# Kernel optimization log

Measured on AMD Instinct MI355X. Metric: run time of the kernel, lower is better.

The kernel has to match this reference:

```python
import jax, jax.numpy as jnp
import numpy as np

JITTER_EPS = 0.01  # router_jitter_noise


def sparsemixer_top2(scores, jitter_eps):
    # scores: [T, E]. Faithful port of PhiMoE sparsemixer (top_k == 2).
    E = scores.shape[-1]
    eye = jnp.arange(E)
    # ---- expert 1 ----
    max1 = jnp.max(scores, axis=-1, keepdims=True)
    ind1 = jnp.argmax(scores, axis=-1)                      # [T]
    factor1 = jnp.maximum(jnp.abs(scores), max1)            # scores.abs().clamp(min=max)
    mask1 = (max1 - scores) / factor1 > 2.0 * jitter_eps
    gates1 = jax.nn.softmax(jnp.where(mask1, -jnp.inf, scores), axis=-1)
    mult1 = jnp.take_along_axis(gates1, ind1[:, None], axis=-1)   # [T,1]
    # ---- expert 2: mask out first pick, repeat ----
    oh1 = eye[None, :] == ind1[:, None]
    masked_scores = jnp.where(oh1, -jnp.inf, scores)
    max2 = jnp.max(masked_scores, axis=-1, keepdims=True)
    ind2 = jnp.argmax(masked_scores, axis=-1)
    factor2 = jnp.maximum(jnp.abs(scores), max2)
    mask2 = (max2 - scores) / factor2 > 2.0 * jitter_eps
    gates2 = jax.nn.softmax(jnp.where(mask2, -jnp.inf, masked_scores), axis=-1)
    mult2 = jnp.take_along_axis(gates2, ind2[:, None], axis=-1)   # [T,1]
    topk_w = jnp.concatenate([mult1, mult2], axis=-1)       # [T,2]
    topk_ids = jnp.stack([ind1, ind2], axis=-1)             # [T,2]
    return topk_w, topk_ids


def setup_inputs() -> dict:
    key = jax.random.key(0)
    ks = jax.random.split(key, 5)
    B, S, D, F, E = 2, 2048, 1024, 2048, 8
    hidden_states = jax.random.normal(ks[0], (B, S, D), dtype=jnp.float32)
    gate_w = jax.random.normal(ks[1], (E, D), dtype=jnp.float32) * (D ** -0.5)
    w_gate = jax.random.normal(ks[2], (E, F, D), dtype=jnp.float32) * (D ** -0.5)
    w_up = jax.random.normal(ks[3], (E, F, D), dtype=jnp.float32) * (D ** -0.5)
    w_down = jax.random.normal(ks[4], (E, D, F), dtype=jnp.float32) * (F ** -0.5)
    return {"hidden_states": hidden_states, "gate_w": gate_w,
            "w_gate": w_gate, "w_up": w_up, "w_down": w_down}


def reference(hidden_states, gate_w, w_gate, w_up, w_down):
    B, S, D = hidden_states.shape
    E = gate_w.shape[0]
    x = hidden_states.reshape(-1, D)                         # [T,D]
    router_logits = x @ gate_w.T                             # [T,E]
    topk_w, topk_ids = sparsemixer_top2(router_logits, JITTER_EPS)
    # per-token combine weights over experts: [T,E]
    comb = jnp.sum(topk_w[:, :, None] *
                   (topk_ids[:, :, None] == jnp.arange(E)[None, None, :]).astype(topk_w.dtype),
                   axis=1)
    out = jnp.zeros_like(x)
    for e in range(E):  # small fixed expert count
        h = jax.nn.silu(x @ w_gate[e].T) * (x @ w_up[e].T)   # [T,F]
        out = out + comb[:, e:e + 1] * (h @ w_down[e].T)     # [T,D]
    return out.reshape(B, S, D), router_logits
```

## Files before the change

kernel.cpp:

```cpp
#include <hip/hip_runtime.h>
#include <stdint.h>

#define TOK    4096
#define DMODEL 1024
#define FDIM   2048
#define NEXP   8
#define MAXP   9216
#define MAXT   72
#define OUT_MAIN (TOK * DMODEL)

#define IDX_NT  24
#define IDX_TE  32
#define IDX_TR  112

#define OFF_META 0
#define OFF_TKW  33792
#define OFF_PTOK 66560
#define OFF_PW   103424
#define OFF_XG   140288
#define OFF_H    19014656
#define OFF_WGB  56763392
#define OFF_WUB  90317824
#define OFF_WDB  123872256
#define OFF_PV   OFF_WGB
#define OFF_RPOS 157426688
#define WS_NEED  157459456

typedef __attribute__((ext_vector_type(8)))  __bf16 bf16x8;
typedef __attribute__((ext_vector_type(8)))  unsigned short u16x8;
typedef __attribute__((ext_vector_type(4)))  unsigned short u16x4;
typedef __attribute__((ext_vector_type(16))) float f32x16;

__device__ __forceinline__ unsigned short f2bf(float f) {
  unsigned u = __builtin_bit_cast(unsigned, f);
  u += 0x7fffu + ((u >> 16) & 1u);
  return (unsigned short)(u >> 16);
}

__device__ __forceinline__ void async_load16(const void* g, void* l) {
  __builtin_amdgcn_global_load_lds(
      (__attribute__((address_space(1))) void*)g,
      (__attribute__((address_space(3))) void*)l, 16, 0, 0);
}

__device__ __forceinline__ bf16x8 ld_frag(const unsigned short* p) {
  return __builtin_bit_cast(bf16x8, *(const u16x8*)p);
}

__global__ void k_prep(const float* __restrict__ wg, const float* __restrict__ wu,
                       const float* __restrict__ wd, unsigned short* __restrict__ wgb,
                       unsigned short* __restrict__ wub, unsigned short* __restrict__ wdb,
                       const float* __restrict__ x, const float* __restrict__ gw,
                       float* __restrict__ logits, int pre) {
  int b = blockIdx.x;
  if (b < 24576) {
    if (!pre) return;
    const float* src; unsigned short* dst; int bb;
    if (b < 8192)       { src = wg; dst = wgb; bb = b; }
    else if (b < 16384) { src = wu; dst = wub; bb = b - 8192; }
    else                { src = wd; dst = wdb; bb = b - 16384; }
    size_t i = ((size_t)bb * 256 + threadIdx.x) * 8;
    float4 a = *(const float4*)(src + i);
    float4 c = *(const float4*)(src + i + 4);
    u16x8 v = {f2bf(a.x), f2bf(a.y), f2bf(a.z), f2bf(a.w),
               f2bf(c.x), f2bf(c.y), f2bf(c.z), f2bf(c.w)};
    *(u16x8*)(dst + i) = v;
    return;
  }
  int lane = threadIdx.x & 63;
  int t = (b - 24576) * 4 + (threadIdx.x >> 6);
  double acc[NEXP];
#pragma unroll
  for (int e = 0; e < NEXP; ++e) acc[e] = 0.0;
  const float* xp = x + (size_t)t * DMODEL;
  for (int i = 0; i < DMODEL / 64; ++i) {
    int d = i * 64 + lane;
    float xv = xp[d];
#pragma unroll
    for (int e = 0; e < NEXP; ++e) acc[e] += (double)xv * (double)gw[e * DMODEL + d];
  }
#pragma unroll
  for (int e = 0; e < NEXP; ++e) {
    double v = acc[e];
#pragma unroll
    for (int off = 32; off > 0; off >>= 1) v += __shfl_down(v, off, 64);
    if (lane == 0) logits[t * NEXP + e] = (float)v;
  }
}

__global__ __launch_bounds__(1024) void k_route2(
    const float* __restrict__ logits, int* __restrict__ meta,
    float* __restrict__ tk_w, int* __restrict__ ptok, float* __restrict__ pw,
    int* __restrict__ rpos) {
  __shared__ int cnt[NEXP], cur[NEXP], seg[NEXP];
  int tid = threadIdx.x;
  if (tid < NEXP) { cnt[tid] = 0; cur[tid] = 0; }
  for (int r = tid; r < MAXP; r += 1024) ptok[r] = -1;
  __syncthreads();
  int i1[4], i2[4]; float w1v[4], w2v[4];
#pragma unroll
  for (int j = 0; j < 4; ++j) {
    int t = tid + j * 1024;
    float s[NEXP];
#pragma unroll
    for (int e = 0; e < NEXP; ++e) s[e] = logits[t * NEXP + e];
    float max1 = s[0]; int ind1 = 0;
#pragma unroll
    for (int e = 1; e < NEXP; ++e) if (s[e] > max1) { max1 = s[e]; ind1 = e; }
    float sum1 = 0.f;
#pragma unroll
    for (int e = 0; e < NEXP; ++e) {
      float f = fmaxf(fabsf(s[e]), max1);
      if (!((max1 - s[e]) / f > 0.02f)) sum1 += expf(s[e] - max1);
    }
    float max2 = -3.4e38f; int ind2 = 0;
#pragma unroll
    for (int e = 0; e < NEXP; ++e) if (e != ind1 && s[e] > max2) { max2 = s[e]; ind2 = e; }
    float sum2 = 0.f;
#pragma unroll
    for (int e = 0; e < NEXP; ++e) {
      if (e == ind1) continue;
      float f = fmaxf(fabsf(s[e]), max2);
      if (!((max2 - s[e]) / f > 0.02f)) sum2 += expf(s[e] - max2);
    }
    i1[j] = ind1; i2[j] = ind2; w1v[j] = 1.f / sum1; w2v[j] = 1.f / sum2;
    atomicAdd(&cnt[ind1], 1);
    atomicAdd(&cnt[ind2], 1);
  }
  __syncthreads();
  if (tid == 0) {
    int off = 0, nt2 = 0;
    for (int e = 0; e < NEXP; ++e) {
      seg[e] = off;
      int tiles = (cnt[e] + 127) >> 7;
      for (int j = 0; j < tiles; ++j) {
        meta[IDX_TE + nt2] = e;
        meta[IDX_TR + nt2] = off + (j << 7);
        ++nt2;
      }
      off += tiles << 7;
    }
    meta[IDX_NT] = nt2;
  }
  __syncthreads();
#pragma unroll
  for (int j = 0; j < 4; ++j) {
    int t = tid + j * 1024;
    int e1 = i1[j];
    int p1 = atomicAdd(&cur[e1], 1);
    int r1 = seg[e1] + p1;
    ptok[r1] = t; pw[r1] = w1v[j]; rpos[2 * t] = r1; tk_w[2 * t] = w1v[j];
    int e2 = i2[j];
    int p2 = atomicAdd(&cur[e2], 1);
    int r2 = seg[e2] + p2;
    ptok[r2] = t; pw[r2] = w2v[j]; rpos[2 * t + 1] = r2; tk_w[2 * t + 1] = w2v[j];
  }
}

__global__ void k_gather(const float* __restrict__ x, const int* __restrict__ ptok,
                         unsigned short* __restrict__ xg) {
  int r = blockIdx.x;
  int t = ptok[r];
  int c = threadIdx.x << 2;
  unsigned short o0 = 0, o1 = 0, o2 = 0, o3 = 0;
  if (t >= 0) {
    float4 v = *(const float4*)(x + ((size_t)t << 10) + c);
    o0 = f2bf(v.x); o1 = f2bf(v.y); o2 = f2bf(v.z); o3 = f2bf(v.w);
  }
  u16x4 o = {o0, o1, o2, o3};
  *(u16x4*)(xg + ((size_t)r << 10) + c) = o;
}

template <bool PRE>
__global__ __launch_bounds__(256, 4) void k_gu(
    const unsigned short* __restrict__ xg,
    const float* __restrict__ wg32, const float* __restrict__ wu32,
    const unsigned short* __restrict__ wgb, const unsigned short* __restrict__ wub,
    unsigned short* __restrict__ h, const int* __restrict__ meta) {
  int nt = meta[IDX_NT];
  int rt = blockIdx.y;
  if (rt >= nt) return;
  int e = meta[IDX_TE + rt];
  int row0 = meta[IDX_TR + rt];
  int n0 = blockIdx.x * 64;

  __shared__ __align__(16) unsigned short As[8192], Bg[4096], Bu[4096];

  int tid = threadIdx.x, lane = tid & 63, w = tid >> 6;
  int wm = w & 1, wn = w >> 1;
  int l31 = lane & 31, lh = lane >> 5;

  f32x16 accg[2], accu[2];
#pragma unroll
  for (int i = 0; i < 2; ++i) {
#pragma unroll
    for (int r = 0; r < 16; ++r) { accg[i][r] = 0.f; accu[i][r] = 0.f; }
  }

  const unsigned short* Abase =
      xg + (size_t)(row0 + w * 32 + l31) * DMODEL + lh * 8;
  int c0 = w * 2, c1 = c0 + 1;
  const unsigned short* G0; const unsigned short* G1;
  const unsigned short* U0; const unsigned short* U1;
  if constexpr (PRE) {
    const unsigned short* WgB = wgb + (size_t)e * FDIM * DMODEL;
    const unsigned short* WuB = wub + (size_t)e * FDIM * DMODEL;
    size_t o0 = (size_t)(n0 + ((c0 >> 2) << 5) + l31) * DMODEL + ((c0 & 3) << 4) + lh * 8;
    size_t o1 = (size_t)(n0 + ((c1 >> 2) << 5) + l31) * DMODEL + ((c1 & 3) << 4) + lh * 8;
    G0 = WgB + o0; G1 = WgB + o1; U0 = WuB + o0; U1 = WuB + o1;
  }

  for (int ks = 0; ks < DMODEL / 64; ++ks) {
    int k0 = ks * 64;
    if (ks) __syncthreads();
    async_load16(Abase + k0,      &As[(w * 4 + 0) * 512]);
    async_load16(Abase + k0 + 16, &As[(w * 4 + 1) * 512]);
    async_load16(Abase + k0 + 32, &As[(w * 4 + 2) * 512]);
    async_load16(Abase + k0 + 48, &As[(w * 4 + 3) * 512]);
    if constexpr (PRE) {
      async_load16(G0 + k0, &Bg[c0 * 512]);
      async_load16(G1 + k0, &Bg[c1 * 512]);
      async_load16(U0 + k0, &Bu[c0 * 512]);
      async_load16(U1 + k0, &Bu[c1 * 512]);
    } else {
      const float* Wg = wg32 + (size_t)e * FDIM * DMODEL;
      const float* Wu = wu32 + (size_t)e * FDIM * DMODEL;
#pragma unroll
      for (int i2 = 0; i2 < 2; ++i2) {
        int tau = tid + 256 * i2;
        int c = tau >> 6, l = tau & 63;
        int nrow = n0 + ((c >> 2) << 5) + (l & 31);
        int kk = k0 + ((c & 3) << 4) + ((l >> 5) << 3);
        const float* sg = Wg + (size_t)nrow * DMODEL + kk;
        const float* su = Wu + (size_t)nrow * DMODEL + kk;
        float4 g0 = *(const float4*)sg;
        float4 g1 = *(const float4*)(sg + 4);
        float4 u0 = *(const float4*)su;
        float4 u1 = *(const float4*)(su + 4);
        u16x8 vg = {f2bf(g0.x), f2bf(g0.y), f2bf(g0.z), f2bf(g0.w),
                    f2bf(g1.x), f2bf(g1.y), f2bf(g1.z), f2bf(g1.w)};
        u16x8 vu = {f2bf(u0.x), f2bf(u0.y), f2bf(u0.z), f2bf(u0.w),
                    f2bf(u1.x), f2bf(u1.y), f2bf(u1.z), f2bf(u1.w)};
        *(u16x8*)&Bg[c * 512 + l * 8] = vg;
        *(u16x8*)&Bu[c * 512 + l * 8] = vu;
      }
    }
    __syncthreads();
#pragma unroll
    for (int kq = 0; kq < 4; ++kq) {
      bf16x8 a0 = ld_frag(&As[((wm * 2 + 0) * 4 + kq) * 512 + lane * 8]);
      bf16x8 a1 = ld_frag(&As[((wm * 2 + 1) * 4 + kq) * 512 + lane * 8]);
      bf16x8 vg = ld_frag(&Bg[(wn * 4 + kq) * 512 + lane * 8]);
      bf16x8 vu = ld_frag(&Bu[(wn * 4 + kq) * 512 + lane * 8]);
      accg[0] = __builtin_amdgcn_mfma_f32_32x32x16_bf16(a0, vg, accg[0], 0, 0, 0);
      accg[1] = __builtin_amdgcn_mfma_f32_32x32x16_bf16(a1, vg, accg[1], 0, 0, 0);
      accu[0] = __builtin_amdgcn_mfma_f32_32x32x16_bf16(a0, vu, accu[0], 0, 0, 0);
      accu[1] = __builtin_amdgcn_mfma_f32_32x32x16_bf16(a1, vu, accu[1], 0, 0, 0);
    }
  }
  int col = n0 + wn * 32 + l31;
#pragma unroll
  for (int mt = 0; mt < 2; ++mt) {
#pragma unroll
    for (int r = 0; r < 16; ++r) {
      int lrow = wm * 64 + mt * 32 + (r & 3) + ((r >> 2) << 3) + lh * 4;
      float gv = accg[mt][r], uv = accu[mt][r];
      float hv = gv * uv / (1.f + __expf(-gv));
      h[(size_t)(row0 + lrow) * FDIM + col] = f2bf(hv);
    }
  }
}

template <bool PRE>
__global__ __launch_bounds__(256, 5) void k_down(
    const unsigned short* __restrict__ h, const float* __restrict__ wd32,
    const unsigned short* __restrict__ wdb, float* __restrict__ out,
    float* __restrict__ pv, const int* __restrict__ meta,
    const int* __restrict__ ptok, const float* __restrict__ pw) {
  int nt = meta[IDX_NT];
  int rt = blockIdx.y;
  if (rt >= nt) return;
  int e = meta[IDX_TE + rt];
  int row0 = meta[IDX_TR + rt];
  int d0 = blockIdx.x * 64;

  __shared__ __align__(16) unsigned short Ah[8192], Bd[4096];
  __shared__ int stok[128];
  __shared__ float sw[128];

  int tid = threadIdx.x, lane = tid & 63, w = tid >> 6;
  int wm = w & 1, wn = w >> 1;
  int l31 = lane & 31, lh = lane >> 5;

  if constexpr (!PRE) {
    if (tid < 128) { stok[tid] = ptok[row0 + tid]; sw[tid] = pw[row0 + tid]; }
  }

  f32x16 acc[2];
#pragma unroll
  for (int i = 0; i < 2; ++i) {
#pragma unroll
    for (int r = 0; r < 16; ++r) acc[i][r] = 0.f;
  }

  const unsigned short* Abase =
      h + (size_t)(row0 + w * 32 + l31) * FDIM + lh * 8;
  int c0 = w * 2, c1 = c0 + 1;
  const unsigned short* D0; const unsigned short* D1;
  if constexpr (PRE) {
    const unsigned short* WdB = wdb + (size_t)e * DMODEL * FDIM;
    D0 = WdB + (size_t)(d0 + ((c0 >> 2) << 5) + l31) * FDIM + ((c0 & 3) << 4) + lh * 8;
    D1 = WdB + (size_t)(d0 + ((c1 >> 2) << 5) + l31) * FDIM + ((c1 & 3) << 4) + lh * 8;
  }

  for (int ks = 0; ks < FDIM / 64; ++ks) {
    int k0 = ks * 64;
    if (ks) __syncthreads();
    async_load16(Abase + k0,      &Ah[(w * 4 + 0) * 512]);
    async_load16(Abase + k0 + 16, &Ah[(w * 4 + 1) * 512]);
    async_load16(Abase + k0 + 32, &Ah[(w * 4 + 2) * 512]);
    async_load16(Abase + k0 + 48, &Ah[(w * 4 + 3) * 512]);
    if constexpr (PRE) {
      async_load16(D0 + k0, &Bd[c0 * 512]);
      async_load16(D1 + k0, &Bd[c1 * 512]);
    } else {
      const float* Wd = wd32 + (size_t)e * DMODEL * FDIM;
#pragma unroll
      for (int i2 = 0; i2 < 2; ++i2) {
        int tau = tid + 256 * i2;
        int c = tau >> 6, l = tau & 63;
        int drow = d0 + ((c >> 2) << 5) + (l & 31);
        int kk = k0 + ((c & 3) << 4) + ((l >> 5) << 3);
        const float* sd = Wd + (size_t)drow * FDIM + kk;
        float4 b0 = *(const float4*)sd;
        float4 b1 = *(const float4*)(sd + 4);
        u16x8 vb = {f2bf(b0.x), f2bf(b0.y), f2bf(b0.z), f2bf(b0.w),
                    f2bf(b1.x), f2bf(b1.y), f2bf(b1.z), f2bf(b1.w)};
        *(u16x8*)&Bd[c * 512 + l * 8] = vb;
      }
    }
    __syncthreads();
#pragma unroll
    for (int kq = 0; kq < 4; ++kq) {
      bf16x8 a0 = ld_frag(&Ah[((wm * 2 + 0) * 4 + kq) * 512 + lane * 8]);
      bf16x8 a1 = ld_frag(&Ah[((wm * 2 + 1) * 4 + kq) * 512 + lane * 8]);
      bf16x8 vb = ld_frag(&Bd[(wn * 4 + kq) * 512 + lane * 8]);
      acc[0] = __builtin_amdgcn_mfma_f32_32x32x16_bf16(a0, vb, acc[0], 0, 0, 0);
      acc[1] = __builtin_amdgcn_mfma_f32_32x32x16_bf16(a1, vb, acc[1], 0, 0, 0);
    }
  }
  int col = d0 + wn * 32 + l31;
#pragma unroll
  for (int mt = 0; mt < 2; ++mt) {
#pragma unroll
    for (int r = 0; r < 16; ++r) {
      int lrow = wm * 64 + mt * 32 + (r & 3) + ((r >> 2) << 3) + lh * 4;
      if constexpr (PRE) {
        pv[(size_t)(row0 + lrow) * DMODEL + col] = acc[mt][r];
      } else {
        int t = stok[lrow];
        if (t >= 0) atomicAdd(&out[(size_t)t * DMODEL + col], acc[mt][r] * sw[lrow]);
      }
    }
  }
}

__global__ void k_combine(const float* __restrict__ pv, const int* __restrict__ rpos,
                          const float* __restrict__ tkw, float* __restrict__ out) {
  int t = blockIdx.x;
  int r1 = rpos[2 * t], r2 = rpos[2 * t + 1];
  float w1 = tkw[2 * t], w2 = tkw[2 * t + 1];
  int c = threadIdx.x << 2;
  float4 a = *(const float4*)(pv + (size_t)r1 * DMODEL + c);
  float4 b = *(const float4*)(pv + (size_t)r2 * DMODEL + c);
  float4 o;
  o.x = w1 * a.x + w2 * b.x;
  o.y = w1 * a.y + w2 * b.y;
  o.z = w1 * a.z + w2 * b.z;
  o.w = w1 * a.w + w2 * b.w;
  *(float4*)(out + (size_t)t * DMODEL + c) = o;
}

extern "C" void kernel_launch(void* const* d_in, const int* in_sizes, int n_in,
                              void* d_out, int out_size, void* d_ws, size_t ws_size,
                              hipStream_t stream) {
  const float* x  = (const float*)d_in[0];
  const float* gw = (const float*)d_in[1];
  const float* wg = (const float*)d_in[2];
  const float* wu = (const float*)d_in[3];
  const float* wd = (const float*)d_in[4];
  float* out = (float*)d_out;
  float* logits = out + OUT_MAIN;

  char* wsb = (char*)d_ws;
  int* meta = (int*)(wsb + OFF_META);
  float* tk_w = (float*)(wsb + OFF_TKW);
  int* ptok = (int*)(wsb + OFF_PTOK);
  float* pw = (float*)(wsb + OFF_PW);
  unsigned short* xg = (unsigned short*)(wsb + OFF_XG);
  unsigned short* h = (unsigned short*)(wsb + OFF_H);
  unsigned short* wgb = (unsigned short*)(wsb + OFF_WGB);
  unsigned short* wub = (unsigned short*)(wsb + OFF_WUB);
  unsigned short* wdb = (unsigned short*)(wsb + OFF_WDB);
  float* pv = (float*)(wsb + OFF_PV);
  int* rpos = (int*)(wsb + OFF_RPOS);

  bool pre = ws_size >= (size_t)WS_NEED;
  if (!pre) hipMemsetAsync(out, 0, (size_t)OUT_MAIN * sizeof(float), stream);

  k_prep<<<25600, 256, 0, stream>>>(wg, wu, wd, wgb, wub, wdb, x, gw, logits, (int)pre);
  k_route2<<<1, 1024, 0, stream>>>(logits, meta, tk_w, ptok, pw, rpos);
  k_gather<<<MAXP, 256, 0, stream>>>(x, ptok, xg);
  if (pre) {
    k_gu<true><<<dim3(FDIM / 64, MAXT), 256, 0, stream>>>(xg, wg, wu, wgb, wub, h, meta);
    k_down<true><<<dim3(DMODEL / 64, MAXT), 256, 0, stream>>>(h, wd, wdb, out, pv, meta, ptok, pw);
    k_combine<<<TOK, 256, 0, stream>>>(pv, rpos, tk_w, out);
  } else {
    k_gu<false><<<dim3(FDIM / 64, MAXT), 256, 0, stream>>>(xg, wg, wu, wgb, wub, h, meta);
    k_down<false><<<dim3(DMODEL / 64, MAXT), 256, 0, stream>>>(h, wd, wdb, out, pv, meta, ptok, pw);
  }
}
```

Measured before the change: 519.2 us.

## Enlarge MoE GEMM tiles to 256x128 with 512-thread blocks and double-buffered LDS

The gate/up and down expert GEMMs move from 128x64 tiles with 256 threads to 256x128 tiles with 512 threads. Each wave now holds four M sub-tiles, which raises operand reuse per LDS fragment. The K loop is double-buffered so the next slab's async loads overlap the current MFMA work. Routing now pads each expert segment to multiples of 256 rows, so the workspace layout and MAXP/MAXT change to match. In exchange there is more padded work per expert, and the larger LDS footprint (about 128KB for gate/up) likely limits each CU to one block.

```diff
diff --git a/kernel.cpp b/kernel.cpp
--- a/kernel.cpp
+++ b/kernel.cpp
@@ -5,8 +5,8 @@
 #define DMODEL 1024
 #define FDIM   2048
 #define NEXP   8
-#define MAXP   9216
-#define MAXT   72
+#define MAXP   10240
+#define MAXT   40
 #define OUT_MAIN (TOK * DMODEL)
 
 #define IDX_NT  24
@@ -16,15 +16,15 @@
 #define OFF_META 0
 #define OFF_TKW  33792
 #define OFF_PTOK 66560
-#define OFF_PW   103424
-#define OFF_XG   140288
-#define OFF_H    19014656
-#define OFF_WGB  56763392
-#define OFF_WUB  90317824
-#define OFF_WDB  123872256
+#define OFF_PW   107520
+#define OFF_XG   148480
+#define OFF_H    21120000
+#define OFF_WGB  63063040
+#define OFF_WUB  96617472
+#define OFF_WDB  130171904
 #define OFF_PV   OFF_WGB
-#define OFF_RPOS 157426688
-#define WS_NEED  157459456
+#define OFF_RPOS 163726336
+#define WS_NEED  163759104
 
 typedef __attribute__((ext_vector_type(8)))  __bf16 bf16x8;
 typedef __attribute__((ext_vector_type(8)))  unsigned short u16x8;
@@ -132,13 +132,13 @@
     int off = 0, nt2 = 0;
     for (int e = 0; e < NEXP; ++e) {
       seg[e] = off;
-      int tiles = (cnt[e] + 127) >> 7;
+      int tiles = (cnt[e] + 255) >> 8;
       for (int j = 0; j < tiles; ++j) {
         meta[IDX_TE + nt2] = e;
-        meta[IDX_TR + nt2] = off + (j << 7);
+        meta[IDX_TR + nt2] = off + (j << 8);
         ++nt2;
       }
-      off += tiles << 7;
+      off += tiles << 8;
     }
     meta[IDX_NT] = nt2;
   }
@@ -172,7 +172,7 @@
 }
 
 template <bool PRE>
-__global__ __launch_bounds__(256, 4) void k_gu(
+__global__ __launch_bounds__(512, 2) void k_gu(
     const unsigned short* __restrict__ xg,
     const float* __restrict__ wg32, const float* __restrict__ wu32,
     const unsigned short* __restrict__ wgb, const unsigned short* __restrict__ wub,
@@ -182,52 +182,55 @@
   if (rt >= nt) return;
   int e = meta[IDX_TE + rt];
   int row0 = meta[IDX_TR + rt];
-  int n0 = blockIdx.x * 64;
-
-  __shared__ __align__(16) unsigned short As[8192], Bg[4096], Bu[4096];
+  int n0 = blockIdx.x * 128;
+
+  __shared__ __align__(16) unsigned short sA[2][16384];
+  __shared__ __align__(16) unsigned short sBg[2][8192];
+  __shared__ __align__(16) unsigned short sBu[2][8192];
 
   int tid = threadIdx.x, lane = tid & 63, w = tid >> 6;
   int wm = w & 1, wn = w >> 1;
   int l31 = lane & 31, lh = lane >> 5;
 
-  f32x16 accg[2], accu[2];
-#pragma unroll
-  for (int i = 0; i < 2; ++i) {
-#pragma unroll
-    for (int r = 0; r < 16; ++r) { accg[i][r] = 0.f; accu[i][r] = 0.f; }
+  f32x16 accg[4], accu[4];
+#pragma unroll
+  for (int m = 0; m < 4; ++m) {
+#pragma unroll
+    for (int r = 0; r < 16; ++r) { accg[m][r] = 0.f; accu[m][r] = 0.f; }
   }
 
   const unsigned short* Abase =
       xg + (size_t)(row0 + w * 32 + l31) * DMODEL + lh * 8;
-  int c0 = w * 2, c1 = c0 + 1;
-  const unsigned short* G0; const unsigned short* G1;
-  const unsigned short* U0; const unsigned short* U1;
+  int cb0 = w * 2, cb1 = cb0 + 1;
+  const unsigned short *G0, *G1, *U0, *U1;
   if constexpr (PRE) {
     const unsigned short* WgB = wgb + (size_t)e * FDIM * DMODEL;
     const unsigned short* WuB = wub + (size_t)e * FDIM * DMODEL;
-    size_t o0 = (size_t)(n0 + ((c0 >> 2) << 5) + l31) * DMODEL + ((c0 & 3) << 4) + lh * 8;
-    size_t o1 = (size_t)(n0 + ((c1 >> 2) << 5) + l31) * DMODEL + ((c1 & 3) << 4) + lh * 8;
+    size_t o0 = (size_t)(n0 + ((cb0 >> 2) << 5) + l31) * DMODEL + ((cb0 & 3) << 4) + lh * 8;
+    size_t o1 = (size_t)(n0 + ((cb1 >> 2) << 5) + l31) * DMODEL + ((cb1 & 3) << 4) + lh * 8;
     G0 = WgB + o0; G1 = WgB + o1; U0 = WuB + o0; U1 = WuB + o1;
   }
-
-  for (int ks = 0; ks < DMODEL / 64; ++ks) {
+  const float* Wg = nullptr; const float* Wu = nullptr;
+  if constexpr (!PRE) {
+    Wg = wg32 + (size_t)e * FDIM * DMODEL;
+    Wu = wu32 + (size_t)e * FDIM * DMODEL;
+  }
+
+  auto stage = [&](int buf, int ks) {
     int k0 = ks * 64;
-    if (ks) __syncthreads();
-    async_load16(Abase + k0,      &As[(w * 4 + 0) * 512]);
-    async_load16(Abase + k0 + 16, &As[(w * 4 + 1) * 512]);
-    async_load16(Abase + k0 + 32, &As[(w * 4 + 2) * 512]);
-    async_load16(Abase + k0 + 48, &As[(w * 4 + 3) * 512]);
+    async_load16(Abase + k0,      &sA[buf][(w * 4 + 0) * 512]);
+    async_load16(Abase + k0 + 16, &sA[buf][(w * 4 + 1) * 512]);
+    async_load16(Abase + k0 + 32, &sA[buf][(w * 4 + 2) * 512]);
+    async_load16(Abase + k0 + 48, &sA[buf][(w * 4 + 3) * 512]);
     if constexpr (PRE) {
-      async_load16(G0 + k0, &Bg[c0 * 512]);
-      async_load16(G1 + k0, &Bg[c1 * 512]);
-      async_load16(U0 + k0, &Bu[c0 * 512]);
-      async_load16(U1 + k0, &Bu[c1 * 512]);
+      async_load16(G0 + k0, &sBg[buf][cb0 * 512]);
+      async_load16(G1 + k0, &sBg[buf][cb1 * 512]);
+      async_load16(U0 + k0, &sBu[buf][cb0 * 512]);
+      async_load16(U1 + k0, &sBu[buf][cb1 * 512]);
     } else {
-      const float* Wg = wg32 + (size_t)e * FDIM * DMODEL;
-      const float* Wu = wu32 + (size_t)e * FDIM * DMODEL;
 #pragma unroll
       for (int i2 = 0; i2 < 2; ++i2) {
-        int tau = tid + 256 * i2;
+        int tau = tid + 512 * i2;
         int c = tau >> 6, l = tau & 63;
         int nrow = n0 + ((c >> 2) << 5) + (l & 31);
         int kk = k0 + ((c & 3) << 4) + ((l >> 5) << 3);
@@ -241,30 +244,49 @@
                     f2bf(g1.x), f2bf(g1.y), f2bf(g1.z), f2bf(g1.w)};
         u16x8 vu = {f2bf(u0.x), f2bf(u0.y), f2bf(u0.z), f2bf(u0.w),
                     f2bf(u1.x), f2bf(u1.y), f2bf(u1.z), f2bf(u1.w)};
-        *(u16x8*)&Bg[c * 512 + l * 8] = vg;
-        *(u16x8*)&Bu[c * 512 + l * 8] = vu;
+        *(u16x8*)&sBg[buf][c * 512 + l * 8] = vg;
+        *(u16x8*)&sBu[buf][c * 512 + l * 8] = vu;
       }
     }
-    __syncthreads();
+  };
+
+  auto compute = [&](int buf) {
 #pragma unroll
     for (int kq = 0; kq < 4; ++kq) {
-      bf16x8 a0 = ld_frag(&As[((wm * 2 + 0) * 4 + kq) * 512 + lane * 8]);
-      bf16x8 a1 = ld_frag(&As[((wm * 2 + 1) * 4 + kq) * 512 + lane * 8]);
-      bf16x8 vg = ld_frag(&Bg[(wn * 4 + kq) * 512 + lane * 8]);
-      bf16x8 vu = ld_frag(&Bu[(wn * 4 + kq) * 512 + lane * 8]);
+      bf16x8 a0 = ld_frag(&sA[buf][((wm * 4 + 0) * 4 + kq) * 512 + lane * 8]);
+      bf16x8 a1 = ld_frag(&sA[buf][((wm * 4 + 1) * 4 + kq) * 512 + lane * 8]);
+      bf16x8 a2 = ld_frag(&sA[buf][((wm * 4 + 2) * 4 + kq) * 512 + lane * 8]);
+      bf16x8 a3 = ld_frag(&sA[buf][((wm * 4 + 3) * 4 + kq) * 512 + lane * 8]);
+      bf16x8 vg = ld_frag(&sBg[buf][(wn * 4 + kq) * 512 + lane * 8]);
+      bf16x8 vu = ld_frag(&sBu[buf][(wn * 4 + kq) * 512 + lane * 8]);
       accg[0] = __builtin_amdgcn_mfma_f32_32x32x16_bf16(a0, vg, accg[0], 0, 0, 0);
       accg[1] = __builtin_amdgcn_mfma_f32_32x32x16_bf16(a1, vg, accg[1], 0, 0, 0);
+      accg[2] = __builtin_amdgcn_mfma_f32_32x32x16_bf16(a2, vg, accg[2], 0, 0, 0);
+      accg[3] = __builtin_amdgcn_mfma_f32_32x32x16_bf16(a3, vg, accg[3], 0, 0, 0);
       accu[0] = __builtin_amdgcn_mfma_f32_32x32x16_bf16(a0, vu, accu[0], 0, 0, 0);
       accu[1] = __builtin_amdgcn_mfma_f32_32x32x16_bf16(a1, vu, accu[1], 0, 0, 0);
-    }
-  }
+      accu[2] = __builtin_amdgcn_mfma_f32_32x32x16_bf16(a2, vu, accu[2], 0, 0, 0);
+      accu[3] = __builtin_amdgcn_mfma_f32_32x32x16_bf16(a3, vu, accu[3], 0, 0, 0);
+    }
+  };
+
+  stage(0, 0);
+  __syncthreads();
+  int cur = 0;
+  for (int ks = 0; ks < DMODEL / 64; ++ks) {
+    if (ks + 1 < DMODEL / 64) stage(cur ^ 1, ks + 1);
+    compute(cur);
+    __syncthreads();
+    cur ^= 1;
+  }
+
   int col = n0 + wn * 32 + l31;
 #pragma unroll
-  for (int mt = 0; mt < 2; ++mt) {
+  for (int m = 0; m < 4; ++m) {
 #pragma unroll
     for (int r = 0; r < 16; ++r) {
-      int lrow = wm * 64 + mt * 32 + (r & 3) + ((r >> 2) << 3) + lh * 4;
-      float gv = accg[mt][r], uv = accu[mt][r];
+      int lrow = wm * 128 + m * 32 + (r & 3) + ((r >> 2) << 3) + lh * 4;
+      float gv = accg[m][r], uv = accu[m][r];
       float hv = gv * uv / (1.f + __expf(-gv));
       h[(size_t)(row0 + lrow) * FDIM + col] = f2bf(hv);
     }
@@ -272,7 +294,7 @@
 }
 
 template <bool PRE>
-__global__ __launch_bounds__(256, 5) void k_down(
+__global__ __launch_bounds__(512, 2) void k_down(
     const unsigned short* __restrict__ h, const float* __restrict__ wd32,
     const unsigned short* __restrict__ wdb, float* __restrict__ out,
     float* __restrict__ pv, const int* __restrict__ meta,
@@ -282,52 +304,53 @@
   if (rt >= nt) return;
   int e = meta[IDX_TE + rt];
   int row0 = meta[IDX_TR + rt];
-  int d0 = blockIdx.x * 64;
-
-  __shared__ __align__(16) unsigned short Ah[8192], Bd[4096];
-  __shared__ int stok[128];
-  __shared__ float sw[128];
+  int d0 = blockIdx.x * 128;
+
+  __shared__ __align__(16) unsigned short sA[2][16384];
+  __shared__ __align__(16) unsigned short sB[2][8192];
+  __shared__ int stok[256];
+  __shared__ float sw_[256];
 
   int tid = threadIdx.x, lane = tid & 63, w = tid >> 6;
   int wm = w & 1, wn = w >> 1;
   int l31 = lane & 31, lh = lane >> 5;
 
   if constexpr (!PRE) {
-    if (tid < 128) { stok[tid] = ptok[row0 + tid]; sw[tid] = pw[row0 + tid]; }
-  }
-
-  f32x16 acc[2];
-#pragma unroll
-  for (int i = 0; i < 2; ++i) {
-#pragma unroll
-    for (int r = 0; r < 16; ++r) acc[i][r] = 0.f;
+    if (tid < 256) { stok[tid] = ptok[row0 + tid]; sw_[tid] = pw[row0 + tid]; }
+  }
+
+  f32x16 acc[4];
+#pragma unroll
+  for (int m = 0; m < 4; ++m) {
+#pragma unroll
+    for (int r = 0; r < 16; ++r) acc[m][r] = 0.f;
   }
 
   const unsigned short* Abase =
       h + (size_t)(row0 + w * 32 + l31) * FDIM + lh * 8;
-  int c0 = w * 2, c1 = c0 + 1;
-  const unsigned short* D0; const unsigned short* D1;
+  int cb0 = w * 2, cb1 = cb0 + 1;
+  const unsigned short *D0, *D1;
   if constexpr (PRE) {
     const unsigned short* WdB = wdb + (size_t)e * DMODEL * FDIM;
-    D0 = WdB + (size_t)(d0 + ((c0 >> 2) << 5) + l31) * FDIM + ((c0 & 3) << 4) + lh * 8;
-    D1 = WdB + (size_t)(d0 + ((c1 >> 2) << 5) + l31) * FDIM + ((c1 & 3) << 4) + lh * 8;
-  }
-
-  for (int ks = 0; ks < FDIM / 64; ++ks) {
+    D0 = WdB + (size_t)(d0 + ((cb0 >> 2) << 5) + l31) * FDIM + ((cb0 & 3) << 4) + lh * 8;
+    D1 = WdB + (size_t)(d0 + ((cb1 >> 2) << 5) + l31) * FDIM + ((cb1 & 3) << 4) + lh * 8;
+  }
+  const float* Wd = nullptr;
+  if constexpr (!PRE) Wd = wd32 + (size_t)e * DMODEL * FDIM;
+
+  auto stage = [&](int buf, int ks) {
     int k0 = ks * 64;
-    if (ks) __syncthreads();
-    async_load16(Abase + k0,      &Ah[(w * 4 + 0) * 512]);
-    async_load16(Abase + k0 + 16, &Ah[(w * 4 + 1) * 512]);
-    async_load16(Abase + k0 + 32, &Ah[(w * 4 + 2) * 512]);
-    async_load16(Abase + k0 + 48, &Ah[(w * 4 + 3) * 512]);
+    async_load16(Abase + k0,      &sA[buf][(w * 4 + 0) * 512]);
+    async_load16(Abase + k0 + 16, &sA[buf][(w * 4 + 1) * 512]);
+    async_load16(Abase + k0 + 32, &sA[buf][(w * 4 + 2) * 512]);
+    async_load16(Abase + k0 + 48, &sA[buf][(w * 4 + 3) * 512]);
     if constexpr (PRE) {
-      async_load16(D0 + k0, &Bd[c0 * 512]);
-      async_load16(D1 + k0, &Bd[c1 * 512]);
+      async_load16(D0 + k0, &sB[buf][cb0 * 512]);
+      async_load16(D1 + k0, &sB[buf][cb1 * 512]);
     } else {
-      const float* Wd = wd32 + (size_t)e * DMODEL * FDIM;
 #pragma unroll
       for (int i2 = 0; i2 < 2; ++i2) {
-        int tau = tid + 256 * i2;
+        int tau = tid + 512 * i2;
         int c = tau >> 6, l = tau & 63;
         int drow = d0 + ((c >> 2) << 5) + (l & 31);
         int kk = k0 + ((c & 3) << 4) + ((l >> 5) << 3);
@@ -336,30 +359,47 @@
         float4 b1 = *(const float4*)(sd + 4);
         u16x8 vb = {f2bf(b0.x), f2bf(b0.y), f2bf(b0.z), f2bf(b0.w),
                     f2bf(b1.x), f2bf(b1.y), f2bf(b1.z), f2bf(b1.w)};
-        *(u16x8*)&Bd[c * 512 + l * 8] = vb;
+        *(u16x8*)&sB[buf][c * 512 + l * 8] = vb;
       }
     }
-    __syncthreads();
+  };
+
+  auto compute = [&](int buf) {
 #pragma unroll
     for (int kq = 0; kq < 4; ++kq) {
-      bf16x8 a0 = ld_frag(&Ah[((wm * 2 + 0) * 4 + kq) * 512 + lane * 8]);
-      bf16x8 a1 = ld_frag(&Ah[((wm * 2 + 1) * 4 + kq) * 512 + lane * 8]);
-      bf16x8 vb = ld_frag(&Bd[(wn * 4 + kq) * 512 + lane * 8]);
+      bf16x8 a0 = ld_frag(&sA[buf][((wm * 4 + 0) * 4 + kq) * 512 + lane * 8]);
+      bf16x8 a1 = ld_frag(&sA[buf][((wm * 4 + 1) * 4 + kq) * 512 + lane * 8]);
+      bf16x8 a2 = ld_frag(&sA[buf][((wm * 4 + 2) * 4 + kq) * 512 + lane * 8]);
+      bf16x8 a3 = ld_frag(&sA[buf][((wm * 4 + 3) * 4 + kq) * 512 + lane * 8]);
+      bf16x8 vb = ld_frag(&sB[buf][(wn * 4 + kq) * 512 + lane * 8]);
       acc[0] = __builtin_amdgcn_mfma_f32_32x32x16_bf16(a0, vb, acc[0], 0, 0, 0);
       acc[1] = __builtin_amdgcn_mfma_f32_32x32x16_bf16(a1, vb, acc[1], 0, 0, 0);
-    }
-  }
+      acc[2] = __builtin_amdgcn_mfma_f32_32x32x16_bf16(a2, vb, acc[2], 0, 0, 0);
+      acc[3] = __builtin_amdgcn_mfma_f32_32x32x16_bf16(a3, vb, acc[3], 0, 0, 0);
+    }
+  };
+
+  stage(0, 0);
+  __syncthreads();
+  int cur = 0;
+  for (int ks = 0; ks < FDIM / 64; ++ks) {
+    if (ks + 1 < FDIM / 64) stage(cur ^ 1, ks + 1);
+    compute(cur);
+    __syncthreads();
+    cur ^= 1;
+  }
+
   int col = d0 + wn * 32 + l31;
 #pragma unroll
-  for (int mt = 0; mt < 2; ++mt) {
+  for (int m = 0; m < 4; ++m) {
 #pragma unroll
     for (int r = 0; r < 16; ++r) {
-      int lrow = wm * 64 + mt * 32 + (r & 3) + ((r >> 2) << 3) + lh * 4;
+      int lrow = wm * 128 + m * 32 + (r & 3) + ((r >> 2) << 3) + lh * 4;
       if constexpr (PRE) {
-        pv[(size_t)(row0 + lrow) * DMODEL + col] = acc[mt][r];
+        pv[(size_t)(row0 + lrow) * DMODEL + col] = acc[m][r];
       } else {
         int t = stok[lrow];
-        if (t >= 0) atomicAdd(&out[(size_t)t * DMODEL + col], acc[mt][r] * sw[lrow]);
+        if (t >= 0) atomicAdd(&out[(size_t)t * DMODEL + col], acc[m][r] * sw_[lrow]);
       }
     }
   }
@@ -412,11 +452,11 @@
   k_route2<<<1, 1024, 0, stream>>>(logits, meta, tk_w, ptok, pw, rpos);
   k_gather<<<MAXP, 256, 0, stream>>>(x, ptok, xg);
   if (pre) {
-    k_gu<true><<<dim3(FDIM / 64, MAXT), 256, 0, stream>>>(xg, wg, wu, wgb, wub, h, meta);
-    k_down<true><<<dim3(DMODEL / 64, MAXT), 256, 0, stream>>>(h, wd, wdb, out, pv, meta, ptok, pw);
+    k_gu<true><<<dim3(FDIM / 128, MAXT), 512, 0, stream>>>(xg, wg, wu, wgb, wub, h, meta);
+    k_down<true><<<dim3(DMODEL / 128, MAXT), 512, 0, stream>>>(h, wd, wdb, out, pv, meta, ptok, pw);
     k_combine<<<TOK, 256, 0, stream>>>(pv, rpos, tk_w, out);
   } else {
-    k_gu<false><<<dim3(FDIM / 64, MAXT), 256, 0, stream>>>(xg, wg, wu, wgb, wub, h, meta);
-    k_down<false><<<dim3(DMODEL / 64, MAXT), 256, 0, stream>>>(h, wd, wdb, out, pv, meta, ptok, pw);
-  }
-}
+    k_gu<false><<<dim3(FDIM / 128, MAXT), 512, 0, stream>>>(xg, wg, wu, wgb, wub, h, meta);
+    k_down<false><<<dim3(DMODEL / 128, MAXT), 512, 0, stream>>>(h, wd, wdb, out, pv, meta, ptok, pw);
+  }
+}
```

Result: slower. 559.0 us (+7.7%).
